# Optimization experiments

Measured on AMD Instinct MI355X. Metric: run time of the kernel, lower is better.

The kernel has to match this reference:

```python
import jax, jax.numpy as jnp
import numpy as np

B, L, H, E, NH = 4, 1024, 1024, 16, 16
D = H // NH  # head_dim = 64; expert hidden == intermediate == D


def setup_inputs() -> dict:
    key = jax.random.key(0)
    ks = jax.random.split(key, 10)
    f32 = jnp.float32
    x = jax.random.normal(ks[0], (B, L, H), dtype=f32)
    # multi_head_layer: Linear(H, H) stored as [in, out] for x @ W + b
    Wmh = jax.random.normal(ks[1], (H, H), dtype=f32) * 0.02
    bmh = jnp.zeros((H,), dtype=f32)
    # router expert embedding [head_dim, E] (nn.Parameter(torch.randn(...)))
    expert_emb = jax.random.normal(ks[2], (D, E), dtype=f32)
    # stacked expert weights (E experts, each SwiGLU-ish MLP of D->D)
    w1 = jax.random.normal(ks[3], (E, D, D), dtype=f32) * 0.05
    b1 = jnp.zeros((E, D), dtype=f32)
    w2 = jax.random.normal(ks[4], (E, D, D), dtype=f32) * 0.05
    b2 = jnp.zeros((E, D), dtype=f32)
    w3 = jax.random.normal(ks[5], (E, D, D), dtype=f32) * 0.05
    b3 = jnp.zeros((E, D), dtype=f32)
    # merge_layer: Linear(H, H)
    Wm = jax.random.normal(ks[6], (H, H), dtype=f32) * 0.02
    bm = jnp.zeros((H,), dtype=f32)
    return {"x": x, "Wmh": Wmh, "bmh": bmh, "expert_emb": expert_emb,
            "w1": w1, "b1": b1, "w2": w2, "b2": b2, "w3": w3, "b3": b3,
            "Wm": Wm, "bm": bm, "topk": 2}


def reference(x, Wmh, bmh, expert_emb, w1, b1, w2, b2, w3, b3, Wm, bm, topk):
    bs, seq, hid = x.shape
    nh = NH
    hd = hid // nh
    # multi-head projection, then split each token into nh sub-tokens
    h = x @ Wmh + bmh                       # [B, L, H]
    h = h.reshape(bs * seq * nh, hd)        # [N, D]
    # router: softmax over experts, then top-k (weights NOT renormalized,
    # matching the torch code which takes topk of the softmax directly)
    logits = h @ expert_emb                 # [N, E]
    probs = jax.nn.softmax(logits, axis=-1)
    rw, sel = jax.lax.top_k(probs, topk)    # [N, k], [N, k]
    # dense all-expert MLP (faithful to torch: every expert on every token)
    # note: Expert applies relu(w1), relu(w2), then w3 (layer_norm unused)
    eo = jax.nn.relu(jnp.einsum('nd,edf->nef', h, w1) + b1[None])   # [N, E, D]
    eo = jax.nn.relu(jnp.einsum('nef,efg->neg', eo, w2) + b2[None]) # [N, E, D]
    eo = jnp.einsum('neg,egh->neh', eo, w3) + b3[None]              # [N, E, D]
    # gather top-k experts per sub-token and combine
    selo = jnp.take_along_axis(eo, sel[:, :, None], axis=1)         # [N, k, D]
    comb = jnp.sum(selo * rw[:, :, None], axis=1)                   # [N, D]
    out = comb.reshape(bs, seq, nh * hd)
    return out @ Wm + bm
```

## Files before the change

### kernel.cpp

```cpp
#include <hip/hip_runtime.h>
#include <hip/hip_bf16.h>

#define MTOK   4096
#define HID    1024
#define NSUB   65536
#define DDIM   64
#define NEXP   16

#define CAP    NSUB
#define T_TILE 64

#define KSTR   40

typedef float  f32x4  __attribute__((ext_vector_type(4)));
typedef short  s16x8  __attribute__((ext_vector_type(8)));

static __device__ __forceinline__ unsigned short f2bf(float f) {
    union { float f; unsigned u; } c; c.f = f;
    return (unsigned short)((c.u + 0x7fffu + ((c.u >> 16) & 1u)) >> 16);
}

template <bool COMBINE>
__global__ __launch_bounds__(256) void sgemm128(
    const float* __restrict__ A, const float* __restrict__ A2,
    const float* __restrict__ Bw, const float* __restrict__ bias,
    float* __restrict__ C, int M, int N, int K)
{
    __shared__ float As[16][132];
    __shared__ float Bs[16][128];

    const int tid = threadIdx.x;
    const int bm = blockIdx.y * 128;
    const int bn = blockIdx.x * 128;
    const int tx = tid & 15;
    const int ty = tid >> 4;

    const int a_kq = (tid & 3) * 4;
    const int a_r  = tid >> 2;
    const int b_nq = (tid & 31) * 4;
    const int b_k  = tid >> 5;

    float acc[8][8];
#pragma unroll
    for (int i = 0; i < 8; i++)
#pragma unroll
        for (int j = 0; j < 8; j++) acc[i][j] = 0.f;

    float4 ra[2], ra2[2], rb[2];
#pragma unroll
    for (int rr = 0; rr < 2; rr++) {
        const int row = bm + a_r + rr * 64;
        ra[rr] = *(const float4*)&A[(size_t)row * K + a_kq];
        if (COMBINE) ra2[rr] = *(const float4*)&A2[(size_t)row * K + a_kq];
    }
#pragma unroll
    for (int kk = 0; kk < 2; kk++) {
        const int k = b_k + kk * 8;
        rb[kk] = *(const float4*)&Bw[(size_t)k * N + bn + b_nq];
    }

    const int ntiles = K / 16;
    for (int t = 0; t < ntiles; t++) {
#pragma unroll
        for (int rr = 0; rr < 2; rr++) {
            float4 v = ra[rr];
            if (COMBINE) { v.x += ra2[rr].x; v.y += ra2[rr].y;
                           v.z += ra2[rr].z; v.w += ra2[rr].w; }
            const int row = a_r + rr * 64;
            As[a_kq + 0][row] = v.x; As[a_kq + 1][row] = v.y;
            As[a_kq + 2][row] = v.z; As[a_kq + 3][row] = v.w;
        }
#pragma unroll
        for (int kk = 0; kk < 2; kk++)
            *(float4*)&Bs[b_k + kk * 8][b_nq] = rb[kk];
        __syncthreads();

        if (t + 1 < ntiles) {
            const int k0 = (t + 1) * 16;
#pragma unroll
            for (int rr = 0; rr < 2; rr++) {
                const int row = bm + a_r + rr * 64;
                ra[rr] = *(const float4*)&A[(size_t)row * K + k0 + a_kq];
                if (COMBINE) ra2[rr] = *(const float4*)&A2[(size_t)row * K + k0 + a_kq];
            }
#pragma unroll
            for (int kk = 0; kk < 2; kk++) {
                const int k = b_k + kk * 8;
                rb[kk] = *(const float4*)&Bw[(size_t)(k0 + k) * N + bn + b_nq];
            }
        }

#pragma unroll
        for (int k = 0; k < 16; k++) {
            float a[8], b[8];
            *(float4*)&a[0] = *(const float4*)&As[k][ty * 4];
            *(float4*)&a[4] = *(const float4*)&As[k][ty * 4 + 64];
            *(float4*)&b[0] = *(const float4*)&Bs[k][tx * 4];
            *(float4*)&b[4] = *(const float4*)&Bs[k][tx * 4 + 64];
#pragma unroll
            for (int i = 0; i < 8; i++)
#pragma unroll
                for (int j = 0; j < 8; j++)
                    acc[i][j] = fmaf(a[i], b[j], acc[i][j]);
        }
        __syncthreads();
    }

#pragma unroll
    for (int i = 0; i < 8; i++) {
        const int row = bm + ty * 4 + (i & 3) + (i >> 2) * 64;
#pragma unroll
        for (int jg = 0; jg < 2; jg++) {
            const int col = bn + tx * 4 + jg * 64;
            float4 v;
            v.x = acc[i][jg * 4 + 0] + bias[col + 0];
            v.y = acc[i][jg * 4 + 1] + bias[col + 1];
            v.z = acc[i][jg * 4 + 2] + bias[col + 2];
            v.w = acc[i][jg * 4 + 3] + bias[col + 3];
            *(float4*)&C[(size_t)row * N + col] = v;
        }
    }
}

__global__ void zero_cnt(int* __restrict__ cnt) { cnt[threadIdx.x] = 0; }

__global__ __launch_bounds__(256) void router_kernel(
    const float* __restrict__ h, const float* __restrict__ emb,
    float2* __restrict__ rw, int* __restrict__ cnt, int* __restrict__ lists)
{
    __shared__ float es[DDIM][NEXP];
    __shared__ int lcnt[NEXP], gbase[NEXP];
    const int tid = threadIdx.x;
    for (int i = tid; i < DDIM * NEXP; i += 256) ((float*)es)[i] = emb[i];
    if (tid < NEXP) lcnt[tid] = 0;
    __syncthreads();

    const int n = blockIdx.x * 256 + tid;
    const float* hr = h + (size_t)n * DDIM;

    float lg[NEXP];
#pragma unroll
    for (int e = 0; e < NEXP; e++) lg[e] = 0.f;
    for (int i = 0; i < DDIM; i += 4) {
        const float4 hv = *(const float4*)&hr[i];
#pragma unroll
        for (int e = 0; e < NEXP; e++) {
            lg[e] = fmaf(hv.x, es[i + 0][e], lg[e]);
            lg[e] = fmaf(hv.y, es[i + 1][e], lg[e]);
            lg[e] = fmaf(hv.z, es[i + 2][e], lg[e]);
            lg[e] = fmaf(hv.w, es[i + 3][e], lg[e]);
        }
    }
    float m = lg[0];
#pragma unroll
    for (int e = 1; e < NEXP; e++) m = fmaxf(m, lg[e]);
    float p[NEXP], den = 0.f;
#pragma unroll
    for (int e = 0; e < NEXP; e++) { p[e] = expf(lg[e] - m); den += p[e]; }
    int i1 = 0; float v1 = p[0];
#pragma unroll
    for (int e = 1; e < NEXP; e++) if (p[e] > v1) { v1 = p[e]; i1 = e; }
    int i2 = (i1 == 0) ? 1 : 0; float v2 = p[i2];
#pragma unroll
    for (int e = 0; e < NEXP; e++)
        if (e != i1 && e != ((i1 == 0) ? 1 : 0) && p[e] > v2) { v2 = p[e]; i2 = e; }

    const float invd = 1.f / den;
    rw[n] = make_float2(v1 * invd, v2 * invd);

    const int lp1 = atomicAdd(&lcnt[i1], 1);
    const int lp2 = atomicAdd(&lcnt[i2], 1);
    __syncthreads();
    if (tid < NEXP) gbase[tid] = atomicAdd(&cnt[tid], lcnt[tid]);
    __syncthreads();
    lists[i1 * CAP + gbase[i1] + lp1] = n;
    lists[i2 * CAP + gbase[i2] + lp2] = n | 0x10000;
}

__global__ __launch_bounds__(256) void expert_gemm(
    const float* __restrict__ h, const int* __restrict__ cnt,
    const int* __restrict__ lists, const float2* __restrict__ rw,
    const float* __restrict__ w1, const float* __restrict__ b1,
    const float* __restrict__ w2, const float* __restrict__ b2,
    const float* __restrict__ w3, const float* __restrict__ b3,
    float* __restrict__ pa, float* __restrict__ pb)
{
    const int e    = blockIdx.x;
    const int base = blockIdx.y * T_TILE;
    const int ne   = cnt[e];
    if (base >= ne) return;
    const int nt = min(T_TILE, ne - base);

    __shared__ float act0[T_TILE][DDIM];
    __shared__ float act1[T_TILE][DDIM];
    __shared__ int   toks[T_TILE];

    const int tid  = threadIdx.x;
    const int wave = tid >> 6;
    const int lane = tid & 63;
    const int jA   = lane & 31;
    const int half = lane >> 5;

    if (tid < T_TILE) toks[tid] = (tid < nt) ? lists[e * CAP + base + tid] : 0;
    __syncthreads();

#pragma unroll
    for (int p = 0; p < T_TILE / 16; p++) {
        const int r = p * 16 + (tid >> 4);
        const int c = (tid & 15) * 4;
        if (r < nt) {
            const int t = toks[r] & 0xffff;
            *(float4*)&act0[r][c] = *(const float4*)&h[(size_t)t * DDIM + c];
        }
    }
    __syncthreads();

    float wa[DDIM], wb[DDIM];

#define LOAD_W(WP, BP, BA, BB) do {                                          \
        const float* wp_ = (WP) + (size_t)e * DDIM * DDIM;                   \
        _Pragma("unroll")                                                    \
        for (int i = 0; i < DDIM; i++) {                                     \
            wa[i] = wp_[i * DDIM + jA];                                      \
            wb[i] = wp_[i * DDIM + jA + 32];                                 \
        }                                                                    \
        BA = (BP)[e * DDIM + jA]; BB = (BP)[e * DDIM + jA + 32];             \
    } while (0)

#define DOT2(SRC, TR, AA, BB2) do {                                          \
        float a0 = 0.f, a1s = 0.f, b0 = 0.f, b1s = 0.f;                      \
        _Pragma("unroll")                                                    \
        for (int i = 0; i < 32; i += 4) {                                    \
            const float4 v = *(const float4*)&SRC[TR][i];                    \
            a0 = fmaf(v.x, wa[i + 0], a0); b0 = fmaf(v.x, wb[i + 0], b0);    \
            a0 = fmaf(v.y, wa[i + 1], a0); b0 = fmaf(v.y, wb[i + 1], b0);    \
            a0 = fmaf(v.z, wa[i + 2], a0); b0 = fmaf(v.z, wb[i + 2], b0);    \
            a0 = fmaf(v.w, wa[i + 3], a0); b0 = fmaf(v.w, wb[i + 3], b0);    \
        }                                                                    \
        _Pragma("unroll")                                                    \
        for (int i = 32; i < 64; i += 4) {                                   \
            const float4 v = *(const float4*)&SRC[TR][i];                    \
            a1s = fmaf(v.x, wa[i + 0], a1s); b1s = fmaf(v.x, wb[i + 0], b1s);\
            a1s = fmaf(v.y, wa[i + 1], a1s); b1s = fmaf(v.y, wb[i + 1], b1s);\
            a1s = fmaf(v.z, wa[i + 2], a1s); b1s = fmaf(v.z, wb[i + 2], b1s);\
            a1s = fmaf(v.w, wa[i + 3], a1s); b1s = fmaf(v.w, wb[i + 3], b1s);\
        }                                                                    \
        AA = a0 + a1s; BB2 = b0 + b1s;                                       \
    } while (0)

    float ba, bb;
    LOAD_W(w1, b1, ba, bb);
#pragma unroll
    for (int p = 0; p < T_TILE / 8; p++) {
        const int tr = p * 8 + wave * 2 + half;
        float aA, aB;
        DOT2(act0, tr, aA, aB);
        act1[tr][jA]      = fmaxf(aA + ba, 0.f);
        act1[tr][jA + 32] = fmaxf(aB + bb, 0.f);
    }
    LOAD_W(w2, b2, ba, bb);
#pragma unroll
    for (int p = 0; p < T_TILE / 8; p++) {
        const int tr = p * 8 + wave * 2 + half;
        float aA, aB;
        DOT2(act1, tr, aA, aB);
        act0[tr][jA]      = fmaxf(aA + ba, 0.f);
        act0[tr][jA + 32] = fmaxf(aB + bb, 0.f);
    }
    LOAD_W(w3, b3, ba, bb);
#pragma unroll
    for (int p = 0; p < T_TILE / 8; p++) {
        const int tr = p * 8 + wave * 2 + half;
        float aA, aB;
        DOT2(act0, tr, aA, aB);
        if (tr < nt) {
            const int en = toks[tr];
            const int t  = en & 0xffff;
            const float2 wv = rw[t];
            const float wgt = (en & 0x10000) ? wv.y : wv.x;
            float* dst = (en & 0x10000) ? pb : pa;
            dst[(size_t)t * DDIM + jA]      = (aA + ba) * wgt;
            dst[(size_t)t * DDIM + jA + 32] = (aB + bb) * wgt;
        }
    }
#undef LOAD_W
#undef DOT2
}

__global__ __launch_bounds__(256) void transpose_bf16(
    const float* __restrict__ W, unsigned short* __restrict__ WT, int K, int N)
{
    __shared__ float tile[64][65];
    const int k0 = blockIdx.x * 64;
    const int n0 = blockIdx.y * 64;
    const int tid = threadIdx.x;
    const int tr = tid >> 4;
    const int tc = (tid & 15) * 4;
#pragma unroll
    for (int p = 0; p < 4; p++) {
        const int r = p * 16 + tr;
        const float4 v = *(const float4*)&W[(size_t)(k0 + r) * N + n0 + tc];
        tile[r][tc + 0] = v.x; tile[r][tc + 1] = v.y;
        tile[r][tc + 2] = v.z; tile[r][tc + 3] = v.w;
    }
    __syncthreads();
#pragma unroll
    for (int p = 0; p < 4; p++) {
        const int n = p * 16 + tr;
        ushort4 o;
        o.x = f2bf(tile[tc + 0][n]); o.y = f2bf(tile[tc + 1][n]);
        o.z = f2bf(tile[tc + 2][n]); o.w = f2bf(tile[tc + 3][n]);
        *(ushort4*)&WT[(size_t)(n0 + n) * K + k0 + tc] = o;
    }
}

__global__ __launch_bounds__(256) void gemm2_mfma(
    const float* __restrict__ pa, const float* __restrict__ pb,
    const unsigned short* __restrict__ WT, const float* __restrict__ bias,
    float* __restrict__ C, int M, int N, int K)
{
    __shared__ unsigned short A_bf[128][KSTR];
    __shared__ unsigned short B_bf[128][KSTR];

    const int tid  = threadIdx.x;
    const int bm   = blockIdx.y * 128;
    const int bn   = blockIdx.x * 128;
    const int wave = tid >> 6;
    const int lane = tid & 63;
    const int wm   = (wave >> 1) * 64;
    const int wn   = (wave & 1) * 64;
    const int r16  = lane & 15;
    const int g8   = (lane >> 4) * 8;

    const int srow = tid >> 1;
    const int skh  = (tid & 1) * 16;

    f32x4 acc[4][4];
#pragma unroll
    for (int i = 0; i < 4; i++)
#pragma unroll
        for (int j = 0; j < 4; j++) acc[i][j] = (f32x4){0.f, 0.f, 0.f, 0.f};

    for (int k0 = 0; k0 < K; k0 += 32) {
        {
            const float* pA = pa + (size_t)(bm + srow) * K + k0 + skh;
            const float* pB = pb + (size_t)(bm + srow) * K + k0 + skh;
            unsigned short tmp[16];
#pragma unroll
            for (int q = 0; q < 4; q++) {
                const float4 va = *(const float4*)&pA[q * 4];
                const float4 vb = *(const float4*)&pB[q * 4];
                tmp[q * 4 + 0] = f2bf(va.x + vb.x);
                tmp[q * 4 + 1] = f2bf(va.y + vb.y);
                tmp[q * 4 + 2] = f2bf(va.z + vb.z);
                tmp[q * 4 + 3] = f2bf(va.w + vb.w);
            }
            *(s16x8*)&A_bf[srow][skh]     = *(s16x8*)&tmp[0];
            *(s16x8*)&A_bf[srow][skh + 8] = *(s16x8*)&tmp[8];
        }
        {
            const unsigned short* pW = WT + (size_t)(bn + srow) * K + k0 + skh;
            *(s16x8*)&B_bf[srow][skh]     = *(const s16x8*)&pW[0];
            *(s16x8*)&B_bf[srow][skh + 8] = *(const s16x8*)&pW[8];
        }
        __syncthreads();

        s16x8 av[4], bv[4];
#pragma unroll
        for (int i = 0; i < 4; i++)
            av[i] = *(s16x8*)&A_bf[wm + i * 16 + r16][g8];
#pragma unroll
        for (int j = 0; j < 4; j++)
            bv[j] = *(s16x8*)&B_bf[wn + j * 16 + r16][g8];
#pragma unroll
        for (int i = 0; i < 4; i++)
#pragma unroll
            for (int j = 0; j < 4; j++)
                acc[i][j] = __builtin_amdgcn_mfma_f32_16x16x32_bf16(
                    av[i], bv[j], acc[i][j], 0, 0, 0);
        __syncthreads();
    }

#pragma unroll
    for (int i = 0; i < 4; i++)
#pragma unroll
        for (int j = 0; j < 4; j++) {
            const int col = bn + wn + j * 16 + r16;
            const float bv2 = bias[col];
#pragma unroll
            for (int r = 0; r < 4; r++) {
                const int row = bm + wm + i * 16 + (lane >> 4) * 4 + r;
                C[(size_t)row * N + col] = acc[i][j][r] + bv2;
            }
        }
}

extern "C" void kernel_launch(void* const* d_in, const int* in_sizes, int n_in,
                              void* d_out, int out_size, void* d_ws, size_t ws_size,
                              hipStream_t stream)
{
    const float* x    = (const float*)d_in[0];
    const float* Wmh  = (const float*)d_in[1];
    const float* bmh  = (const float*)d_in[2];
    const float* emb  = (const float*)d_in[3];
    const float* w1   = (const float*)d_in[4];
    const float* b1   = (const float*)d_in[5];
    const float* w2   = (const float*)d_in[6];
    const float* b2   = (const float*)d_in[7];
    const float* w3   = (const float*)d_in[8];
    const float* b3   = (const float*)d_in[9];
    const float* Wm   = (const float*)d_in[10];
    const float* bm   = (const float*)d_in[11];
    float* out = (float*)d_out;

    char* ws = (char*)d_ws;
    float*  h     = (float*)(ws);
    float*  pa    = (float*)(ws + (size_t)(16 << 20));
    float*  pb    = (float*)(ws + (size_t)(32 << 20));
    float2* rwp   = (float2*)(ws + (size_t)(48 << 20));
    int*    cntp  = (int*)  (ws + (size_t)(48 << 20) + (NSUB * 8));
    unsigned short* WmT = (unsigned short*)(ws);
    int*    lists = (int*)  d_out;

    sgemm128<false><<<dim3(HID / 128, MTOK / 128), 256, 0, stream>>>(
        x, nullptr, Wmh, bmh, h, MTOK, HID, HID);

    zero_cnt<<<1, NEXP, 0, stream>>>(cntp);
    router_kernel<<<NSUB / 256, 256, 0, stream>>>(h, emb, rwp, cntp, lists);

    expert_gemm<<<dim3(NEXP, CAP / T_TILE), 256, 0, stream>>>(
        h, cntp, lists, rwp, w1, b1, w2, b2, w3, b3, pa, pb);

    transpose_bf16<<<dim3(HID / 64, HID / 64), 256, 0, stream>>>(
        Wm, WmT, HID, HID);

    gemm2_mfma<<<dim3(HID / 128, MTOK / 128), 256, 0, stream>>>(
        pa, pb, WmT, bm, out, MTOK, HID, HID);
}
```

Baseline: 404.2 us.

## Use bf16 MFMA for first projection and fold router into precomputed Wmh·emb

Replaces the fp32 SIMT first GEMM with the bf16 MFMA GEMM, templated to take a single input, and adds a bf16 transpose of Wmh. Router logits are now computed from x against a precomputed F = Wmh_head·emb (plus bias row) in fp32, instead of from h. This keeps expert selection at fp32 precision even though h itself is now produced in bf16. The cost is an extra 1024x256 prep kernel plus a K=1024 per-subtoken router loop that re-reads x rows.

Result: slower. 525.7 us (+30.1%).

```diff
diff --git a/kernel.cpp b/kernel.cpp
--- a/kernel.cpp
+++ b/kernel.cpp
@@ -20,137 +20,61 @@
     return (unsigned short)((c.u + 0x7fffu + ((c.u >> 16) & 1u)) >> 16);
 }
 
-template <bool COMBINE>
-__global__ __launch_bounds__(256) void sgemm128(
-    const float* __restrict__ A, const float* __restrict__ A2,
-    const float* __restrict__ Bw, const float* __restrict__ bias,
-    float* __restrict__ C, int M, int N, int K)
-{
-    __shared__ float As[16][132];
-    __shared__ float Bs[16][128];
-
-    const int tid = threadIdx.x;
-    const int bm = blockIdx.y * 128;
-    const int bn = blockIdx.x * 128;
-    const int tx = tid & 15;
-    const int ty = tid >> 4;
-
-    const int a_kq = (tid & 3) * 4;
-    const int a_r  = tid >> 2;
-    const int b_nq = (tid & 31) * 4;
-    const int b_k  = tid >> 5;
-
-    float acc[8][8];
-#pragma unroll
-    for (int i = 0; i < 8; i++)
-#pragma unroll
-        for (int j = 0; j < 8; j++) acc[i][j] = 0.f;
-
-    float4 ra[2], ra2[2], rb[2];
-#pragma unroll
-    for (int rr = 0; rr < 2; rr++) {
-        const int row = bm + a_r + rr * 64;
-        ra[rr] = *(const float4*)&A[(size_t)row * K + a_kq];
-        if (COMBINE) ra2[rr] = *(const float4*)&A2[(size_t)row * K + a_kq];
-    }
-#pragma unroll
-    for (int kk = 0; kk < 2; kk++) {
-        const int k = b_k + kk * 8;
-        rb[kk] = *(const float4*)&Bw[(size_t)k * N + bn + b_nq];
-    }
-
-    const int ntiles = K / 16;
-    for (int t = 0; t < ntiles; t++) {
-#pragma unroll
-        for (int rr = 0; rr < 2; rr++) {
-            float4 v = ra[rr];
-            if (COMBINE) { v.x += ra2[rr].x; v.y += ra2[rr].y;
-                           v.z += ra2[rr].z; v.w += ra2[rr].w; }
-            const int row = a_r + rr * 64;
-            As[a_kq + 0][row] = v.x; As[a_kq + 1][row] = v.y;
-            As[a_kq + 2][row] = v.z; As[a_kq + 3][row] = v.w;
-        }
-#pragma unroll
-        for (int kk = 0; kk < 2; kk++)
-            *(float4*)&Bs[b_k + kk * 8][b_nq] = rb[kk];
-        __syncthreads();
-
-        if (t + 1 < ntiles) {
-            const int k0 = (t + 1) * 16;
-#pragma unroll
-            for (int rr = 0; rr < 2; rr++) {
-                const int row = bm + a_r + rr * 64;
-                ra[rr] = *(const float4*)&A[(size_t)row * K + k0 + a_kq];
-                if (COMBINE) ra2[rr] = *(const float4*)&A2[(size_t)row * K + k0 + a_kq];
-            }
-#pragma unroll
-            for (int kk = 0; kk < 2; kk++) {
-                const int k = b_k + kk * 8;
-                rb[kk] = *(const float4*)&Bw[(size_t)(k0 + k) * N + bn + b_nq];
-            }
-        }
-
-#pragma unroll
-        for (int k = 0; k < 16; k++) {
-            float a[8], b[8];
-            *(float4*)&a[0] = *(const float4*)&As[k][ty * 4];
-            *(float4*)&a[4] = *(const float4*)&As[k][ty * 4 + 64];
-            *(float4*)&b[0] = *(const float4*)&Bs[k][tx * 4];
-            *(float4*)&b[4] = *(const float4*)&Bs[k][tx * 4 + 64];
-#pragma unroll
-            for (int i = 0; i < 8; i++)
-#pragma unroll
-                for (int j = 0; j < 8; j++)
-                    acc[i][j] = fmaf(a[i], b[j], acc[i][j]);
-        }
-        __syncthreads();
-    }
-
-#pragma unroll
-    for (int i = 0; i < 8; i++) {
-        const int row = bm + ty * 4 + (i & 3) + (i >> 2) * 64;
-#pragma unroll
-        for (int jg = 0; jg < 2; jg++) {
-            const int col = bn + tx * 4 + jg * 64;
-            float4 v;
-            v.x = acc[i][jg * 4 + 0] + bias[col + 0];
-            v.y = acc[i][jg * 4 + 1] + bias[col + 1];
-            v.z = acc[i][jg * 4 + 2] + bias[col + 2];
-            v.w = acc[i][jg * 4 + 3] + bias[col + 3];
-            *(float4*)&C[(size_t)row * N + col] = v;
-        }
-    }
-}
-
 __global__ void zero_cnt(int* __restrict__ cnt) { cnt[threadIdx.x] = 0; }
 
-__global__ __launch_bounds__(256) void router_kernel(
-    const float* __restrict__ h, const float* __restrict__ emb,
+__global__ __launch_bounds__(256) void prep_F(
+    const float* __restrict__ Wmh, const float* __restrict__ bmh,
+    const float* __restrict__ emb, float* __restrict__ F)
+{
+    const int k = blockIdx.x;
+    const int g = threadIdx.x >> 4;
+    const int e = threadIdx.x & 15;
+    const float* src = (k < HID) ? &Wmh[(size_t)k * HID] : bmh;
+    float s = 0.f;
+#pragma unroll
+    for (int d = 0; d < DDIM; d++)
+        s = fmaf(src[g * DDIM + d], emb[d * NEXP + e], s);
+    F[(size_t)k * 256 + threadIdx.x] = s;
+}
+
+__global__ __launch_bounds__(128) void router_F(
+    const float* __restrict__ x, const float* __restrict__ F,
     float2* __restrict__ rw, int* __restrict__ cnt, int* __restrict__ lists)
 {
-    __shared__ float es[DDIM][NEXP];
     __shared__ int lcnt[NEXP], gbase[NEXP];
     const int tid = threadIdx.x;
-    for (int i = tid; i < DDIM * NEXP; i += 256) ((float*)es)[i] = emb[i];
     if (tid < NEXP) lcnt[tid] = 0;
     __syncthreads();
 
-    const int n = blockIdx.x * 256 + tid;
-    const float* hr = h + (size_t)n * DDIM;
+    const int n = blockIdx.x * 128 + tid;
+    const int t = n >> 4;
+    const int g = n & 15;
+    const float* xr = x + (size_t)t * HID;
 
     float lg[NEXP];
-#pragma unroll
-    for (int e = 0; e < NEXP; e++) lg[e] = 0.f;
-    for (int i = 0; i < DDIM; i += 4) {
-        const float4 hv = *(const float4*)&hr[i];
-#pragma unroll
-        for (int e = 0; e < NEXP; e++) {
-            lg[e] = fmaf(hv.x, es[i + 0][e], lg[e]);
-            lg[e] = fmaf(hv.y, es[i + 1][e], lg[e]);
-            lg[e] = fmaf(hv.z, es[i + 2][e], lg[e]);
-            lg[e] = fmaf(hv.w, es[i + 3][e], lg[e]);
-        }
-    }
+    *(float4*)&lg[0]  = *(const float4*)&F[(size_t)HID * 256 + g * 16 + 0];
+    *(float4*)&lg[4]  = *(const float4*)&F[(size_t)HID * 256 + g * 16 + 4];
+    *(float4*)&lg[8]  = *(const float4*)&F[(size_t)HID * 256 + g * 16 + 8];
+    *(float4*)&lg[12] = *(const float4*)&F[(size_t)HID * 256 + g * 16 + 12];
+
+#pragma unroll 4
+    for (int k = 0; k < HID; k++) {
+        const float xv = xr[k];
+        const float* Fr = &F[(size_t)k * 256 + g * 16];
+        const float4 f0 = *(const float4*)&Fr[0];
+        const float4 f1 = *(const float4*)&Fr[4];
+        const float4 f2 = *(const float4*)&Fr[8];
+        const float4 f3 = *(const float4*)&Fr[12];
+        lg[0]  = fmaf(xv, f0.x, lg[0]);  lg[1]  = fmaf(xv, f0.y, lg[1]);
+        lg[2]  = fmaf(xv, f0.z, lg[2]);  lg[3]  = fmaf(xv, f0.w, lg[3]);
+        lg[4]  = fmaf(xv, f1.x, lg[4]);  lg[5]  = fmaf(xv, f1.y, lg[5]);
+        lg[6]  = fmaf(xv, f1.z, lg[6]);  lg[7]  = fmaf(xv, f1.w, lg[7]);
+        lg[8]  = fmaf(xv, f2.x, lg[8]);  lg[9]  = fmaf(xv, f2.y, lg[9]);
+        lg[10] = fmaf(xv, f2.z, lg[10]); lg[11] = fmaf(xv, f2.w, lg[11]);
+        lg[12] = fmaf(xv, f3.x, lg[12]); lg[13] = fmaf(xv, f3.y, lg[13]);
+        lg[14] = fmaf(xv, f3.z, lg[14]); lg[15] = fmaf(xv, f3.w, lg[15]);
+    }
+
     float m = lg[0];
 #pragma unroll
     for (int e = 1; e < NEXP; e++) m = fmaxf(m, lg[e]);
@@ -314,8 +238,9 @@
     }
 }
 
-__global__ __launch_bounds__(256) void gemm2_mfma(
-    const float* __restrict__ pa, const float* __restrict__ pb,
+template <bool COMBINE>
+__global__ __launch_bounds__(256) void gemm_mfma(
+    const float* __restrict__ Aa, const float* __restrict__ Ab,
     const unsigned short* __restrict__ WT, const float* __restrict__ bias,
     float* __restrict__ C, int M, int N, int K)
 {
@@ -343,17 +268,21 @@
 
     for (int k0 = 0; k0 < K; k0 += 32) {
         {
-            const float* pA = pa + (size_t)(bm + srow) * K + k0 + skh;
-            const float* pB = pb + (size_t)(bm + srow) * K + k0 + skh;
+            const float* pA = Aa + (size_t)(bm + srow) * K + k0 + skh;
+            const float* pB = COMBINE ? Ab + (size_t)(bm + srow) * K + k0 + skh
+                                      : nullptr;
             unsigned short tmp[16];
 #pragma unroll
             for (int q = 0; q < 4; q++) {
-                const float4 va = *(const float4*)&pA[q * 4];
-                const float4 vb = *(const float4*)&pB[q * 4];
-                tmp[q * 4 + 0] = f2bf(va.x + vb.x);
-                tmp[q * 4 + 1] = f2bf(va.y + vb.y);
-                tmp[q * 4 + 2] = f2bf(va.z + vb.z);
-                tmp[q * 4 + 3] = f2bf(va.w + vb.w);
+                float4 va = *(const float4*)&pA[q * 4];
+                if constexpr (COMBINE) {
+                    const float4 vb = *(const float4*)&pB[q * 4];
+                    va.x += vb.x; va.y += vb.y; va.z += vb.z; va.w += vb.w;
+                }
+                tmp[q * 4 + 0] = f2bf(va.x);
+                tmp[q * 4 + 1] = f2bf(va.y);
+                tmp[q * 4 + 2] = f2bf(va.z);
+                tmp[q * 4 + 3] = f2bf(va.w);
             }
             *(s16x8*)&A_bf[srow][skh]     = *(s16x8*)&tmp[0];
             *(s16x8*)&A_bf[srow][skh + 8] = *(s16x8*)&tmp[8];
@@ -420,13 +349,21 @@
     float2* rwp   = (float2*)(ws + (size_t)(48 << 20));
     int*    cntp  = (int*)  (ws + (size_t)(48 << 20) + (NSUB * 8));
     unsigned short* WmT = (unsigned short*)(ws);
-    int*    lists = (int*)  d_out;
-
-    sgemm128<false><<<dim3(HID / 128, MTOK / 128), 256, 0, stream>>>(
-        x, nullptr, Wmh, bmh, h, MTOK, HID, HID);
+
+    char* dob = (char*)d_out;
+    int*            lists = (int*)dob;
+    float*          F     = (float*)(dob + (size_t)(8 << 20));
+    unsigned short* WmhT  = (unsigned short*)(dob + (size_t)(12 << 20));
+
+    transpose_bf16<<<dim3(HID / 64, HID / 64), 256, 0, stream>>>(
+        Wmh, WmhT, HID, HID);
+    prep_F<<<HID + 1, 256, 0, stream>>>(Wmh, bmh, emb, F);
+
+    gemm_mfma<false><<<dim3(HID / 128, MTOK / 128), 256, 0, stream>>>(
+        x, nullptr, WmhT, bmh, h, MTOK, HID, HID);
 
     zero_cnt<<<1, NEXP, 0, stream>>>(cntp);
-    router_kernel<<<NSUB / 256, 256, 0, stream>>>(h, emb, rwp, cntp, lists);
+    router_F<<<NSUB / 128, 128, 0, stream>>>(x, F, rwp, cntp, lists);
 
     expert_gemm<<<dim3(NEXP, CAP / T_TILE), 256, 0, stream>>>(
         h, cntp, lists, rwp, w1, b1, w2, b2, w3, b3, pa, pb);
@@ -434,6 +371,6 @@
     transpose_bf16<<<dim3(HID / 64, HID / 64), 256, 0, stream>>>(
         Wm, WmT, HID, HID);
 
-    gemm2_mfma<<<dim3(HID / 128, MTOK / 128), 256, 0, stream>>>(
+    gemm_mfma<true><<<dim3(HID / 128, MTOK / 128), 256, 0, stream>>>(
         pa, pb, WmT, bm, out, MTOK, HID, HID);
 }
```
